# Optimization experiments

Hardware: AMD Instinct MI355X
Metric: run time of the kernel (lower is better)

## Reference

```python
import jax, jax.numpy as jnp
import numpy as np

N = 10000
E = 160000
UNITS = 64
NUM_RBF = 32
CUTOFF = 1.0


def _xavier(k, shape):
    fan_out, fan_in = shape
    lim = float(np.sqrt(6.0 / (fan_in + fan_out)))
    return jax.random.uniform(k, shape, minval=-lim, maxval=lim, dtype=jnp.float32)


def setup_inputs() -> dict:
    key = jax.random.key(0)
    ks = jax.random.split(key, 16)
    inp = {
        "edge_index": jax.random.randint(ks[0], (2, E), 0, N),
        "edge_weight": jax.random.uniform(ks[1], (E,), dtype=jnp.float32),
        "edge_attr": jax.random.normal(ks[2], (E, NUM_RBF), dtype=jnp.float32),
        "X": jax.random.normal(ks[3], (N, UNITS, 3, 3), dtype=jnp.float32),
        # scalar MLP: num_rbf -> units -> 2*units -> 3*units
        "Ws0": _xavier(ks[4], (UNITS, NUM_RBF)), "bs0": jnp.zeros((UNITS,), jnp.float32),
        "Ws1": _xavier(ks[5], (2 * UNITS, UNITS)), "bs1": jnp.zeros((2 * UNITS,), jnp.float32),
        "Ws2": _xavier(ks[6], (3 * UNITS, 2 * UNITS)), "bs2": jnp.zeros((3 * UNITS,), jnp.float32),
    }
    for i in range(6):
        inp[f"Wt{i}"] = _xavier(ks[7 + i], (UNITS, UNITS))
    return inp


def cosine_cutoff(r, cutoff):
    return jnp.where(r < cutoff, 0.5 * (jnp.cos(jnp.pi * r / cutoff) + 1.0), 0.0)


def tensor_norm(X):
    # X: [N, units, 3, 3] -> [N, units]
    return jnp.sum(X * X, axis=(-2, -1))


def decompose_tensor(X):
    eye = jnp.eye(3, dtype=X.dtype)
    trace = jnp.trace(X, axis1=-2, axis2=-1)  # [N, units]
    I = (trace / 3.0)[..., None, None] * eye
    A = 0.5 * (X - jnp.swapaxes(X, -2, -1))
    S = 0.5 * (X + jnp.swapaxes(X, -2, -1)) - I
    return I, A, S


def channel_linear(T, W):
    # linear over the channel dim: [N, c, 3, 3] x [d, c] -> [N, d, 3, 3]
    return jnp.einsum('ncij,dc->ndij', T, W)


def reference(edge_index, edge_weight, edge_attr, X,
              Ws0, bs0, Ws1, bs1, Ws2, bs2,
              Wt0, Wt1, Wt2, Wt3, Wt4, Wt5):
    act = jax.nn.silu
    C = cosine_cutoff(edge_weight, CUTOFF)  # [E]
    h = act(edge_attr @ Ws0.T + bs0)
    h = act(h @ Ws1.T + bs1)
    h = act(h @ Ws2.T + bs2)  # [E, 3*units]
    ea = (h * C[:, None]).reshape(h.shape[0], UNITS, 3)  # [E, units, 3]

    X = X / (tensor_norm(X) + 1.0)[..., None, None]
    I, A, S = decompose_tensor(X)
    I = channel_linear(I, Wt0)
    A = channel_linear(A, Wt1)
    S = channel_linear(S, Wt2)
    Y = I + A + S

    src, dst = edge_index[0], edge_index[1]
    n = X.shape[0]
    # message = per-edge radial scaling of gathered node tensors; aggregate at src
    Im = jax.ops.segment_sum(ea[..., 0, None, None] * I[dst], src, num_segments=n)
    Am = jax.ops.segment_sum(ea[..., 1, None, None] * A[dst], src, num_segments=n)
    Sm = jax.ops.segment_sum(ea[..., 2, None, None] * S[dst], src, num_segments=n)
    msg = Im + Am + Sm

    # O(3): symmetrized product of batched 3x3 matmuls
    AB = jnp.matmul(msg, Y) + jnp.matmul(Y, msg)
    I2, A2, S2 = decompose_tensor(AB)
    normp1 = (tensor_norm(I2 + A2 + S2) + 1.0)[..., None, None]
    I2 = channel_linear(I2 / normp1, Wt3)
    A2 = channel_linear(A2 / normp1, Wt4)
    S2 = channel_linear(S2 / normp1, Wt5)
    dX = I2 + A2 + S2
    return X + dX + jnp.matmul(dX, dX)
```

## Files before the change

### kernel.cpp

```cpp
#include <hip/hip_runtime.h>
#include <math.h>

#define NN 10000
#define EE 160000

#define OFF_WTT 0
#define OFF_PK  24576
#define OFF_B2P 41984
#define OFF_IASH 42176
#define OFF_EAH 3882176
#define OFF_INT 19242176

typedef __attribute__((ext_vector_type(8))) _Float16 h16x8;
typedef __attribute__((ext_vector_type(2))) __fp16 fp16x2_raw;
typedef __attribute__((ext_vector_type(4))) float f32x4;

__device__ __forceinline__ float silu_f(float x) {
    return x * __builtin_amdgcn_rcpf(1.0f + __expf(-x));
}
__device__ __forceinline__ unsigned int pkh(float a, float b) {
    union { fp16x2_raw h; unsigned int u; } cv;
    cv.h = __builtin_amdgcn_cvt_pkrtz(a, b);
    return cv.u;
}
__device__ __forceinline__ unsigned short f2h(float f) {
    union { _Float16 h; unsigned short u; } cv; cv.h = (_Float16)f; return cv.u;
}
__device__ __forceinline__ float h2f(unsigned short s) {
    union { unsigned short u; _Float16 h; } cv; cv.u = s; return (float)cv.h;
}
__device__ __forceinline__ float h2f_lo(unsigned int u) { return h2f((unsigned short)(u & 0xffffu)); }
__device__ __forceinline__ float h2f_hi(unsigned int u) { return h2f((unsigned short)(u >> 16)); }

__global__ void k_prep(const float* __restrict__ Wt0, const float* __restrict__ Wt1,
                       const float* __restrict__ Wt2, const float* __restrict__ Wt3,
                       const float* __restrict__ Wt4, const float* __restrict__ Wt5,
                       const float* __restrict__ Ws0, const float* __restrict__ Ws1,
                       const float* __restrict__ Ws2, const float* __restrict__ bs2,
                       const int* __restrict__ ei,
                       float* __restrict__ WtT, unsigned short* __restrict__ PK,
                       float* __restrict__ bs2p, int* __restrict__ counts) {
    int idx = blockIdx.x * 256 + threadIdx.x;
    if (idx < 24576) {
        int k = idx >> 12, r = idx & 4095;
        int c = r >> 6, d = r & 63;
        const float* W = (k == 0) ? Wt0 : (k == 1) ? Wt1 : (k == 2) ? Wt2
                       : (k == 3) ? Wt3 : (k == 4) ? Wt4 : Wt5;
        WtT[idx] = W[d * 64 + c];
    } else if (idx < 26624) {
        int q = idx - 24576;
        int ot = q >> 9, r = q & 511, lane = r >> 3, j = r & 7;
        int k = ((lane >> 4) * 8) + j, o = ot * 16 + (lane & 15);
        PK[q] = f2h(Ws0[o * 32 + k]);
    } else if (idx < 34816) {
        int q = idx - 24576;
        int i = q - 2048, ch = i >> 9, r = i & 511, lane = r >> 3, j = r & 7;
        int ot = ch >> 1, ks = ch & 1;
        int k = ks * 32 + (lane >> 4) * 8 + j, o = ot * 16 + (lane & 15);
        PK[q] = f2h(Ws1[o * 64 + k]);
    } else if (idx < 59392) {
        int q = idx - 24576;
        int i = q - 10240, ch = i >> 9, r = i & 511, lane = r >> 3, j = r & 7;
        int ot = ch >> 2, ks = ch & 3;
        int k = ks * 32 + (lane >> 4) * 8 + j;
        int op = ot * 16 + (lane & 15);
        int o = (op & 63) * 3 + (op >> 6);
        PK[q] = f2h(Ws2[o * 128 + k]);
    } else if (idx < 59584) {
        int op = idx - 59392;
        bs2p[op] = bs2[(op & 63) * 3 + (op >> 6)];
    } else if (idx < 59584 + EE) {
        int e = idx - 59584;
        atomicAdd(&counts[ei[e]], 1);
    }
}

__global__ __launch_bounds__(256) void k_scan(const int* __restrict__ counts,
                                              int* __restrict__ offsets) {
    __shared__ int sums[256];
    int t = threadIdx.x;
    const int CH = 40;
    int base = t * CH;
    int s = 0;
    for (int i = 0; i < CH; i++) {
        int idx = base + i;
        if (idx < NN) s += counts[idx];
    }
    sums[t] = s;
    __syncthreads();
    for (int off = 1; off < 256; off <<= 1) {
        int tmp = (t >= off) ? sums[t - off] : 0;
        __syncthreads();
        sums[t] += tmp;
        __syncthreads();
    }
    int run = sums[t] - s;
    for (int i = 0; i < CH; i++) {
        int idx = base + i;
        if (idx < NN) { offsets[idx] = run; run += counts[idx]; }
    }
    if (t == 255) offsets[NN] = run;
}

__global__ void k_fill(const int* __restrict__ ei, const int* __restrict__ offsets,
                       int* __restrict__ cursor, int* __restrict__ bucket,
                       int* __restrict__ dstp) {
    int e = blockIdx.x * 256 + threadIdx.x;
    if (e < EE) {
        int s = ei[e];
        int pos = offsets[s] + atomicAdd(&cursor[s], 1);
        bucket[pos] = e;
        dstp[pos] = ei[EE + e];
    }
}

__global__ __launch_bounds__(64) void k_nodeprep(const float* __restrict__ X,
                                                 const float* __restrict__ WtT,
                                                 unsigned short* __restrict__ IASh) {
    int n = blockIdx.x, c = threadIdx.x;
    __shared__ float XS[576];
    __shared__ float L[64][12];
#pragma unroll
    for (int i = 0; i < 9; i++) XS[c + 64 * i] = X[(size_t)n * 576 + c + 64 * i];
    __syncthreads();
    float x[9];
#pragma unroll
    for (int j = 0; j < 9; j++) x[j] = XS[c * 9 + j];
    float nrm = 0.f;
#pragma unroll
    for (int j = 0; j < 9; j++) nrm += x[j] * x[j];
    float inv = __builtin_amdgcn_rcpf(nrm + 1.0f);
#pragma unroll
    for (int j = 0; j < 9; j++) x[j] *= inv;
    float tr3 = (x[0] + x[4] + x[8]) * (1.0f / 3.0f);
    L[c][0] = tr3;
    L[c][1] = 0.5f * (x[1] - x[3]);
    L[c][2] = 0.5f * (x[2] - x[6]);
    L[c][3] = 0.5f * (x[5] - x[7]);
    L[c][4] = x[0] - tr3;
    L[c][5] = x[4] - tr3;
    L[c][6] = 0.5f * (x[1] + x[3]);
    L[c][7] = 0.5f * (x[2] + x[6]);
    L[c][8] = 0.5f * (x[5] + x[7]);
    __syncthreads();
    int d = c;
    const float* W0 = WtT;
    const float* W1 = WtT + 4096;
    const float* W2 = WtT + 8192;
    float aI = 0, aA0 = 0, aA1 = 0, aA2 = 0, aS0 = 0, aS1 = 0, aS2 = 0, aS3 = 0, aS4 = 0;
    for (int cc = 0; cc < 64; ++cc) {
        float w0 = W0[cc * 64 + d], w1 = W1[cc * 64 + d], w2 = W2[cc * 64 + d];
        float4 L0 = *(const float4*)&L[cc][0];
        float4 L1 = *(const float4*)&L[cc][4];
        float L8 = L[cc][8];
        aI  += w0 * L0.x;
        aA0 += w1 * L0.y; aA1 += w1 * L0.z; aA2 += w1 * L0.w;
        aS0 += w2 * L1.x; aS1 += w2 * L1.y; aS2 += w2 * L1.z;
        aS3 += w2 * L1.w; aS4 += w2 * L8;
    }
    unsigned int* op = (unsigned int*)(IASh + (size_t)n * 768 + (size_t)d * 12);
    op[0] = pkh(aI, aA0);
    op[1] = pkh(aA1, aA2);
    op[2] = pkh(aS0, aS1);
    op[3] = pkh(aS2, aS3);
    op[4] = pkh(aS4, 0.0f);
}

__global__ __launch_bounds__(256) void k_mlp(const float* __restrict__ attr,
                                             const float* __restrict__ ew,
                                             const int* __restrict__ bucket,
                                             const unsigned short* __restrict__ PK,
                                             const float* __restrict__ bs0,
                                             const float* __restrict__ bs1,
                                             const float* __restrict__ bs2p,
                                             unsigned short* __restrict__ eah) {
    __shared__ unsigned short H1[64][80];
    __shared__ unsigned short H2[64][144];
    int t = threadIdx.x;
    int e0 = blockIdx.x * 64;
    int l = t & 63, w = t >> 6, rb = w * 16, lr = l & 15, lg = l >> 4;
    int eid = bucket[e0 + rb + lr];
    const float* ap = attr + (size_t)eid * 32 + lg * 8;
    float4 av0 = *(const float4*)ap;
    float4 av1 = *(const float4*)(ap + 4);
    union { h16x8 h; unsigned int u[4]; } B1;
    B1.u[0] = pkh(av0.x, av0.y); B1.u[1] = pkh(av0.z, av0.w);
    B1.u[2] = pkh(av1.x, av1.y); B1.u[3] = pkh(av1.z, av1.w);
    float rw = ew[eid];
    float C = (rw < 1.0f) ? 0.5f * (cosf(3.14159265358979f * rw) + 1.0f) : 0.0f;

    const h16x8* P1 = (const h16x8*)PK;
    const h16x8* P2 = (const h16x8*)(PK + 2048);
    const h16x8* P3 = (const h16x8*)(PK + 10240);

#pragma unroll
    for (int ot = 0; ot < 4; ++ot) {
        float4 bb = *(const float4*)&bs0[ot * 16 + lg * 4];
        f32x4 acc = {bb.x, bb.y, bb.z, bb.w};
        acc = __builtin_amdgcn_mfma_f32_16x16x32_f16(P1[ot * 64 + l], B1.h, acc, 0, 0, 0);
        unsigned int u01 = pkh(silu_f(acc[0]), silu_f(acc[1]));
        unsigned int u23 = pkh(silu_f(acc[2]), silu_f(acc[3]));
        *(uint2*)&H1[rb + lr][ot * 16 + lg * 4] = make_uint2(u01, u23);
    }
    __syncthreads();

    h16x8 B2a = *(const h16x8*)&H1[rb + lr][lg * 8];
    h16x8 B2b = *(const h16x8*)&H1[rb + lr][32 + lg * 8];
#pragma unroll
    for (int ot = 0; ot < 8; ++ot) {
        float4 bb = *(const float4*)&bs1[ot * 16 + lg * 4];
        f32x4 acc = {bb.x, bb.y, bb.z, bb.w};
        acc = __builtin_amdgcn_mfma_f32_16x16x32_f16(P2[(ot * 2 + 0) * 64 + l], B2a, acc, 0, 0, 0);
        acc = __builtin_amdgcn_mfma_f32_16x16x32_f16(P2[(ot * 2 + 1) * 64 + l], B2b, acc, 0, 0, 0);
        unsigned int u01 = pkh(silu_f(acc[0]), silu_f(acc[1]));
        unsigned int u23 = pkh(silu_f(acc[2]), silu_f(acc[3]));
        *(uint2*)&H2[rb + lr][ot * 16 + lg * 4] = make_uint2(u01, u23);
    }
    __syncthreads();

    h16x8 B3[4];
#pragma unroll
    for (int ks = 0; ks < 4; ++ks)
        B3[ks] = *(const h16x8*)&H2[rb + lr][ks * 32 + lg * 8];
    size_t ebase = (size_t)(e0 + rb + lr) * 192;
#pragma unroll
    for (int ot = 0; ot < 12; ++ot) {
        float4 bb = *(const float4*)&bs2p[ot * 16 + lg * 4];
        f32x4 acc = {bb.x, bb.y, bb.z, bb.w};
#pragma unroll
        for (int ks = 0; ks < 4; ++ks)
            acc = __builtin_amdgcn_mfma_f32_16x16x32_f16(P3[(ot * 4 + ks) * 64 + l], B3[ks], acc, 0, 0, 0);
        unsigned int u01 = pkh(silu_f(acc[0]) * C, silu_f(acc[1]) * C);
        unsigned int u23 = pkh(silu_f(acc[2]) * C, silu_f(acc[3]) * C);
        *(uint2*)&eah[ebase + ot * 16 + lg * 4] = make_uint2(u01, u23);
    }
}

__global__ __launch_bounds__(64) void k_aggout(const int* __restrict__ offsets,
                                               const int* __restrict__ dstp,
                                               const unsigned short* __restrict__ eah,
                                               const unsigned short* __restrict__ IASh,
                                               const float* __restrict__ X,
                                               const float* __restrict__ WtT,
                                               float* __restrict__ out) {
    int n = blockIdx.x, c = threadIdx.x;
    __shared__ float XS[576];
    __shared__ float OS[576];
    __shared__ float L[64][12];
#pragma unroll
    for (int i = 0; i < 9; i++) XS[c + 64 * i] = X[(size_t)n * 576 + c + 64 * i];
    __syncthreads();

    int beg = offsets[n], end = offsets[n + 1];
    float m0 = 0, m1 = 0, m2 = 0, m3 = 0, m4 = 0, m5 = 0, m6 = 0, m7 = 0, m8 = 0;
    for (int i = beg; i < end; ++i) {
        int dst = dstp[i];
        const unsigned short* ep = eah + (size_t)i * 192;
        float ea0 = h2f(ep[c]), ea1 = h2f(ep[64 + c]), ea2 = h2f(ep[128 + c]);
        const unsigned int* ip = (const unsigned int*)(IASh + (size_t)dst * 768 + (size_t)c * 12);
        uint2 qa = *(const uint2*)ip;
        uint2 qb = *(const uint2*)(ip + 2);
        unsigned int qc = ip[4];
        m0 += ea0 * h2f_lo(qa.x); m1 += ea1 * h2f_hi(qa.x);
        m2 += ea1 * h2f_lo(qa.y); m3 += ea1 * h2f_hi(qa.y);
        m4 += ea2 * h2f_lo(qb.x); m5 += ea2 * h2f_hi(qb.x);
        m6 += ea2 * h2f_lo(qb.y); m7 += ea2 * h2f_hi(qb.y);
        m8 += ea2 * h2f_lo(qc);
    }
    const unsigned int* yp = (const unsigned int*)(IASh + (size_t)n * 768 + (size_t)c * 12);
    uint2 ya = *(const uint2*)yp;
    uint2 yb = *(const uint2*)(yp + 2);
    unsigned int yc = yp[4];
    float yI = h2f_lo(ya.x), yA0 = h2f_hi(ya.x), yA1 = h2f_lo(ya.y), yA2 = h2f_hi(ya.y);
    float yS0 = h2f_lo(yb.x), yS1 = h2f_hi(yb.x), yS2 = h2f_lo(yb.y), yS3 = h2f_hi(yb.y);
    float yS4 = h2f_lo(yc);

    float M[3][3] = {
        { m0 + m4,   m1 + m6,  m2 + m7 },
        { -m1 + m6,  m0 + m5,  m3 + m8 },
        { -m2 + m7, -m3 + m8,  m0 - m4 - m5 } };
    float Y[3][3] = {
        { yI + yS0,   yA0 + yS2,  yA1 + yS3 },
        { -yA0 + yS2, yI + yS1,   yA2 + yS4 },
        { -yA1 + yS3, -yA2 + yS4, yI - yS0 - yS1 } };
    float AB[3][3];
#pragma unroll
    for (int i = 0; i < 3; i++)
#pragma unroll
        for (int j = 0; j < 3; j++) {
            float s = 0.f;
#pragma unroll
            for (int k = 0; k < 3; k++) s += M[i][k] * Y[k][j] + Y[i][k] * M[k][j];
            AB[i][j] = s;
        }
    float tr3 = (AB[0][0] + AB[1][1] + AB[2][2]) * (1.0f / 3.0f);
    float fro = 0.f;
#pragma unroll
    for (int i = 0; i < 3; i++)
#pragma unroll
        for (int j = 0; j < 3; j++) fro += AB[i][j] * AB[i][j];
    float inv = __builtin_amdgcn_rcpf(fro + 1.0f);
    L[c][0] = tr3 * inv;
    L[c][1] = 0.5f * (AB[0][1] - AB[1][0]) * inv;
    L[c][2] = 0.5f * (AB[0][2] - AB[2][0]) * inv;
    L[c][3] = 0.5f * (AB[1][2] - AB[2][1]) * inv;
    L[c][4] = (AB[0][0] - tr3) * inv;
    L[c][5] = (AB[1][1] - tr3) * inv;
    L[c][6] = 0.5f * (AB[0][1] + AB[1][0]) * inv;
    L[c][7] = 0.5f * (AB[0][2] + AB[2][0]) * inv;
    L[c][8] = 0.5f * (AB[1][2] + AB[2][1]) * inv;
    __syncthreads();
    int d = c;
    const float* W3 = WtT + 3 * 4096;
    const float* W4 = WtT + 4 * 4096;
    const float* W5 = WtT + 5 * 4096;
    float aI = 0, aA0 = 0, aA1 = 0, aA2 = 0, aS0 = 0, aS1 = 0, aS2 = 0, aS3 = 0, aS4 = 0;
    for (int cc = 0; cc < 64; ++cc) {
        float w3 = W3[cc * 64 + d], w4 = W4[cc * 64 + d], w5 = W5[cc * 64 + d];
        float4 L0 = *(const float4*)&L[cc][0];
        float4 L1 = *(const float4*)&L[cc][4];
        float L8 = L[cc][8];
        aI  += w3 * L0.x;
        aA0 += w4 * L0.y; aA1 += w4 * L0.z; aA2 += w4 * L0.w;
        aS0 += w5 * L1.x; aS1 += w5 * L1.y; aS2 += w5 * L1.z;
        aS3 += w5 * L1.w; aS4 += w5 * L8;
    }
    float dX[3][3] = {
        { aI + aS0,   aA0 + aS2,  aA1 + aS3 },
        { -aA0 + aS2, aI + aS1,   aA2 + aS4 },
        { -aA1 + aS3, -aA2 + aS4, aI - aS0 - aS1 } };
    float D2[3][3];
#pragma unroll
    for (int i = 0; i < 3; i++)
#pragma unroll
        for (int j = 0; j < 3; j++) {
            float s = 0.f;
#pragma unroll
            for (int k = 0; k < 3; k++) s += dX[i][k] * dX[k][j];
            D2[i][j] = s;
        }
    float x[9];
#pragma unroll
    for (int j = 0; j < 9; j++) x[j] = XS[d * 9 + j];
    float nrm = 0.f;
#pragma unroll
    for (int j = 0; j < 9; j++) nrm += x[j] * x[j];
    float xinv = __builtin_amdgcn_rcpf(nrm + 1.0f);
#pragma unroll
    for (int i = 0; i < 3; i++)
#pragma unroll
        for (int j = 0; j < 3; j++)
            OS[d * 9 + i * 3 + j] = x[i * 3 + j] * xinv + dX[i][j] + D2[i][j];
    __syncthreads();
#pragma unroll
    for (int i = 0; i < 9; i++) out[(size_t)n * 576 + c + 64 * i] = OS[c + 64 * i];
}

extern "C" void kernel_launch(void* const* d_in, const int* in_sizes, int n_in,
                              void* d_out, int out_size, void* d_ws, size_t ws_size,
                              hipStream_t stream) {
    (void)in_sizes; (void)n_in; (void)out_size; (void)ws_size;
    const int* ei = (const int*)d_in[0];
    const float* ew = (const float*)d_in[1];
    const float* attr = (const float*)d_in[2];
    const float* X = (const float*)d_in[3];
    const float* Ws0 = (const float*)d_in[4];
    const float* bs0 = (const float*)d_in[5];
    const float* Ws1 = (const float*)d_in[6];
    const float* bs1 = (const float*)d_in[7];
    const float* Ws2 = (const float*)d_in[8];
    const float* bs2 = (const float*)d_in[9];
    const float* Wt0 = (const float*)d_in[10];
    const float* Wt1 = (const float*)d_in[11];
    const float* Wt2 = (const float*)d_in[12];
    const float* Wt3 = (const float*)d_in[13];
    const float* Wt4 = (const float*)d_in[14];
    const float* Wt5 = (const float*)d_in[15];
    float* ws = (float*)d_ws;
    int* ibase = (int*)(ws + OFF_INT);
    int* counts = ibase;
    int* cursor = ibase + NN;
    int* offsets = ibase + 2 * NN;
    int* bucket = ibase + 3 * NN + 1;
    int* dstp = bucket + EE;
    unsigned short* PK = (unsigned short*)(ws + OFF_PK);
    unsigned short* IASh = (unsigned short*)(ws + OFF_IASH);
    unsigned short* eah = (unsigned short*)(ws + OFF_EAH);

    (void)hipMemsetAsync(counts, 0, 2 * NN * sizeof(int), stream);
    k_prep<<<(59584 + EE + 255) / 256, 256, 0, stream>>>(
        Wt0, Wt1, Wt2, Wt3, Wt4, Wt5, Ws0, Ws1, Ws2, bs2, ei,
        ws, PK, ws + OFF_B2P, counts);
    k_scan<<<1, 256, 0, stream>>>(counts, offsets);
    k_fill<<<(EE + 255) / 256, 256, 0, stream>>>(ei, offsets, cursor, bucket, dstp);
    k_nodeprep<<<NN, 64, 0, stream>>>(X, ws, IASh);
    k_mlp<<<EE / 64, 256, 0, stream>>>(attr, ew, bucket, PK, bs0, bs1, ws + OFF_B2P, eah);
    k_aggout<<<NN, 64, 0, stream>>>(offsets, dstp, eah, IASh, X, ws, (float*)d_out);
}
```

Measured before the change: 185.7 us.

## Repack node tensors channel-major, pack four nodes per block, vectorize scan

The node-tensor buffer moves from a 12-half-per-channel stride to a channel-major layout of five packed words. Each gathered word is then read coalesced across the wave, and the buffer shrinks from 12 to 10 halves per channel. k_nodeprep and k_aggout now process four nodes per 256-thread block with one wave per node, using wave barriers in place of block syncs. k_mlp drops its block-wide syncs in favour of per-wave shared buffers, the aggregation loop is unrolled by two edges, and the scan reads counts as int4. The cost is more shared memory per block, and correctness now relies on wave-level barriers and on NN being divisible by four.

Result: faster. 162.8 us (-12.3%).

```diff
diff --git a/kernel.cpp b/kernel.cpp
--- a/kernel.cpp
+++ b/kernel.cpp
@@ -8,8 +8,8 @@
 #define OFF_PK  24576
 #define OFF_B2P 41984
 #define OFF_IASH 42176
-#define OFF_EAH 3882176
-#define OFF_INT 19242176
+#define OFF_EAH 3242176
+#define OFF_INT 18602176
 
 typedef __attribute__((ext_vector_type(8))) _Float16 h16x8;
 typedef __attribute__((ext_vector_type(2))) __fp16 fp16x2_raw;
@@ -79,12 +79,12 @@
                                               int* __restrict__ offsets) {
     __shared__ int sums[256];
     int t = threadIdx.x;
-    const int CH = 40;
-    int base = t * CH;
+    int base = t * 40;
     int s = 0;
-    for (int i = 0; i < CH; i++) {
-        int idx = base + i;
-        if (idx < NN) s += counts[idx];
+    if (base < NN) {
+        const int4* p = (const int4*)(counts + base);
+#pragma unroll
+        for (int q = 0; q < 10; ++q) { int4 a = p[q]; s += a.x + a.y + a.z + a.w; }
     }
     sums[t] = s;
     __syncthreads();
@@ -95,9 +95,16 @@
         __syncthreads();
     }
     int run = sums[t] - s;
-    for (int i = 0; i < CH; i++) {
-        int idx = base + i;
-        if (idx < NN) { offsets[idx] = run; run += counts[idx]; }
+    if (base < NN) {
+        const int4* p = (const int4*)(counts + base);
+#pragma unroll
+        for (int q = 0; q < 10; ++q) {
+            int4 a = p[q];
+            offsets[base + 4 * q + 0] = run; run += a.x;
+            offsets[base + 4 * q + 1] = run; run += a.y;
+            offsets[base + 4 * q + 2] = run; run += a.z;
+            offsets[base + 4 * q + 3] = run; run += a.w;
+        }
     }
     if (t == 255) offsets[NN] = run;
 }
@@ -114,18 +121,20 @@
     }
 }
 
-__global__ __launch_bounds__(64) void k_nodeprep(const float* __restrict__ X,
-                                                 const float* __restrict__ WtT,
-                                                 unsigned short* __restrict__ IASh) {
-    int n = blockIdx.x, c = threadIdx.x;
-    __shared__ float XS[576];
-    __shared__ float L[64][12];
-#pragma unroll
-    for (int i = 0; i < 9; i++) XS[c + 64 * i] = X[(size_t)n * 576 + c + 64 * i];
-    __syncthreads();
+__global__ __launch_bounds__(256) void k_nodeprep(const float* __restrict__ X,
+                                                  const float* __restrict__ WtT,
+                                                  unsigned int* __restrict__ IASu) {
+    int t = threadIdx.x, w = t >> 6, c = t & 63;
+    int n = blockIdx.x * 4 + w;
+    __shared__ float XS[4][576];
+    __shared__ float L[4][64][12];
+    float* xs = XS[w];
+#pragma unroll
+    for (int i = 0; i < 9; i++) xs[c + 64 * i] = X[(size_t)n * 576 + c + 64 * i];
+    __builtin_amdgcn_wave_barrier();
     float x[9];
 #pragma unroll
-    for (int j = 0; j < 9; j++) x[j] = XS[c * 9 + j];
+    for (int j = 0; j < 9; j++) x[j] = xs[c * 9 + j];
     float nrm = 0.f;
 #pragma unroll
     for (int j = 0; j < 9; j++) nrm += x[j] * x[j];
@@ -133,16 +142,16 @@
 #pragma unroll
     for (int j = 0; j < 9; j++) x[j] *= inv;
     float tr3 = (x[0] + x[4] + x[8]) * (1.0f / 3.0f);
-    L[c][0] = tr3;
-    L[c][1] = 0.5f * (x[1] - x[3]);
-    L[c][2] = 0.5f * (x[2] - x[6]);
-    L[c][3] = 0.5f * (x[5] - x[7]);
-    L[c][4] = x[0] - tr3;
-    L[c][5] = x[4] - tr3;
-    L[c][6] = 0.5f * (x[1] + x[3]);
-    L[c][7] = 0.5f * (x[2] + x[6]);
-    L[c][8] = 0.5f * (x[5] + x[7]);
-    __syncthreads();
+    L[w][c][0] = tr3;
+    L[w][c][1] = 0.5f * (x[1] - x[3]);
+    L[w][c][2] = 0.5f * (x[2] - x[6]);
+    L[w][c][3] = 0.5f * (x[5] - x[7]);
+    L[w][c][4] = x[0] - tr3;
+    L[w][c][5] = x[4] - tr3;
+    L[w][c][6] = 0.5f * (x[1] + x[3]);
+    L[w][c][7] = 0.5f * (x[2] + x[6]);
+    L[w][c][8] = 0.5f * (x[5] + x[7]);
+    __builtin_amdgcn_wave_barrier();
     int d = c;
     const float* W0 = WtT;
     const float* W1 = WtT + 4096;
@@ -150,20 +159,20 @@
     float aI = 0, aA0 = 0, aA1 = 0, aA2 = 0, aS0 = 0, aS1 = 0, aS2 = 0, aS3 = 0, aS4 = 0;
     for (int cc = 0; cc < 64; ++cc) {
         float w0 = W0[cc * 64 + d], w1 = W1[cc * 64 + d], w2 = W2[cc * 64 + d];
-        float4 L0 = *(const float4*)&L[cc][0];
-        float4 L1 = *(const float4*)&L[cc][4];
-        float L8 = L[cc][8];
+        float4 L0 = *(const float4*)&L[w][cc][0];
+        float4 L1 = *(const float4*)&L[w][cc][4];
+        float L8 = L[w][cc][8];
         aI  += w0 * L0.x;
         aA0 += w1 * L0.y; aA1 += w1 * L0.z; aA2 += w1 * L0.w;
         aS0 += w2 * L1.x; aS1 += w2 * L1.y; aS2 += w2 * L1.z;
         aS3 += w2 * L1.w; aS4 += w2 * L8;
     }
-    unsigned int* op = (unsigned int*)(IASh + (size_t)n * 768 + (size_t)d * 12);
-    op[0] = pkh(aI, aA0);
-    op[1] = pkh(aA1, aA2);
-    op[2] = pkh(aS0, aS1);
-    op[3] = pkh(aS2, aS3);
-    op[4] = pkh(aS4, 0.0f);
+    unsigned int* op = IASu + (size_t)n * 320 + d;
+    op[0]   = pkh(aI, aA0);
+    op[64]  = pkh(aA1, aA2);
+    op[128] = pkh(aS0, aS1);
+    op[192] = pkh(aS2, aS3);
+    op[256] = pkh(aS4, 0.0f);
 }
 
 __global__ __launch_bounds__(256) void k_mlp(const float* __restrict__ attr,
@@ -174,12 +183,11 @@
                                              const float* __restrict__ bs1,
                                              const float* __restrict__ bs2p,
                                              unsigned short* __restrict__ eah) {
-    __shared__ unsigned short H1[64][80];
-    __shared__ unsigned short H2[64][144];
+    __shared__ unsigned short H[4][16][152];
     int t = threadIdx.x;
-    int e0 = blockIdx.x * 64;
-    int l = t & 63, w = t >> 6, rb = w * 16, lr = l & 15, lg = l >> 4;
-    int eid = bucket[e0 + rb + lr];
+    int l = t & 63, w = t >> 6, lr = l & 15, lg = l >> 4;
+    int pos = blockIdx.x * 64 + w * 16 + lr;
+    int eid = bucket[pos];
     const float* ap = attr + (size_t)eid * 32 + lg * 8;
     float4 av0 = *(const float4*)ap;
     float4 av1 = *(const float4*)(ap + 4);
@@ -200,12 +208,13 @@
         acc = __builtin_amdgcn_mfma_f32_16x16x32_f16(P1[ot * 64 + l], B1.h, acc, 0, 0, 0);
         unsigned int u01 = pkh(silu_f(acc[0]), silu_f(acc[1]));
         unsigned int u23 = pkh(silu_f(acc[2]), silu_f(acc[3]));
-        *(uint2*)&H1[rb + lr][ot * 16 + lg * 4] = make_uint2(u01, u23);
-    }
-    __syncthreads();
-
-    h16x8 B2a = *(const h16x8*)&H1[rb + lr][lg * 8];
-    h16x8 B2b = *(const h16x8*)&H1[rb + lr][32 + lg * 8];
+        *(uint2*)&H[w][lr][ot * 16 + lg * 4] = make_uint2(u01, u23);
+    }
+    __builtin_amdgcn_wave_barrier();
+
+    h16x8 B2a = *(const h16x8*)&H[w][lr][lg * 8];
+    h16x8 B2b = *(const h16x8*)&H[w][lr][32 + lg * 8];
+    __builtin_amdgcn_wave_barrier();
 #pragma unroll
     for (int ot = 0; ot < 8; ++ot) {
         float4 bb = *(const float4*)&bs1[ot * 16 + lg * 4];
@@ -214,15 +223,15 @@
         acc = __builtin_amdgcn_mfma_f32_16x16x32_f16(P2[(ot * 2 + 1) * 64 + l], B2b, acc, 0, 0, 0);
         unsigned int u01 = pkh(silu_f(acc[0]), silu_f(acc[1]));
         unsigned int u23 = pkh(silu_f(acc[2]), silu_f(acc[3]));
-        *(uint2*)&H2[rb + lr][ot * 16 + lg * 4] = make_uint2(u01, u23);
-    }
-    __syncthreads();
+        *(uint2*)&H[w][lr][ot * 16 + lg * 4] = make_uint2(u01, u23);
+    }
+    __builtin_amdgcn_wave_barrier();
 
     h16x8 B3[4];
 #pragma unroll
     for (int ks = 0; ks < 4; ++ks)
-        B3[ks] = *(const h16x8*)&H2[rb + lr][ks * 32 + lg * 8];
-    size_t ebase = (size_t)(e0 + rb + lr) * 192;
+        B3[ks] = *(const h16x8*)&H[w][lr][ks * 32 + lg * 8];
+    size_t ebase = (size_t)pos * 192;
 #pragma unroll
     for (int ot = 0; ot < 12; ++ot) {
         float4 bb = *(const float4*)&bs2p[ot * 16 + lg * 4];
@@ -236,44 +245,62 @@
     }
 }
 
-__global__ __launch_bounds__(64) void k_aggout(const int* __restrict__ offsets,
-                                               const int* __restrict__ dstp,
-                                               const unsigned short* __restrict__ eah,
-                                               const unsigned short* __restrict__ IASh,
-                                               const float* __restrict__ X,
-                                               const float* __restrict__ WtT,
-                                               float* __restrict__ out) {
-    int n = blockIdx.x, c = threadIdx.x;
-    __shared__ float XS[576];
-    __shared__ float OS[576];
-    __shared__ float L[64][12];
-#pragma unroll
-    for (int i = 0; i < 9; i++) XS[c + 64 * i] = X[(size_t)n * 576 + c + 64 * i];
-    __syncthreads();
+__global__ __launch_bounds__(256) void k_aggout(const int* __restrict__ offsets,
+                                                const int* __restrict__ dstp,
+                                                const unsigned short* __restrict__ eah,
+                                                const unsigned int* __restrict__ IASu,
+                                                const float* __restrict__ X,
+                                                const float* __restrict__ WtT,
+                                                float* __restrict__ out) {
+    int t = threadIdx.x, w = t >> 6, c = t & 63;
+    int n = blockIdx.x * 4 + w;
+    __shared__ float XS[4][576];
+    __shared__ float LO[4][768];
+    float* xs = XS[w];
+    float* lo = LO[w];
+#pragma unroll
+    for (int i = 0; i < 9; i++) xs[c + 64 * i] = X[(size_t)n * 576 + c + 64 * i];
 
     int beg = offsets[n], end = offsets[n + 1];
     float m0 = 0, m1 = 0, m2 = 0, m3 = 0, m4 = 0, m5 = 0, m6 = 0, m7 = 0, m8 = 0;
-    for (int i = beg; i < end; ++i) {
-        int dst = dstp[i];
-        const unsigned short* ep = eah + (size_t)i * 192;
-        float ea0 = h2f(ep[c]), ea1 = h2f(ep[64 + c]), ea2 = h2f(ep[128 + c]);
-        const unsigned int* ip = (const unsigned int*)(IASh + (size_t)dst * 768 + (size_t)c * 12);
-        uint2 qa = *(const uint2*)ip;
-        uint2 qb = *(const uint2*)(ip + 2);
-        unsigned int qc = ip[4];
-        m0 += ea0 * h2f_lo(qa.x); m1 += ea1 * h2f_hi(qa.x);
-        m2 += ea1 * h2f_lo(qa.y); m3 += ea1 * h2f_hi(qa.y);
-        m4 += ea2 * h2f_lo(qb.x); m5 += ea2 * h2f_hi(qb.x);
-        m6 += ea2 * h2f_lo(qb.y); m7 += ea2 * h2f_hi(qb.y);
-        m8 += ea2 * h2f_lo(qc);
-    }
-    const unsigned int* yp = (const unsigned int*)(IASh + (size_t)n * 768 + (size_t)c * 12);
-    uint2 ya = *(const uint2*)yp;
-    uint2 yb = *(const uint2*)(yp + 2);
-    unsigned int yc = yp[4];
-    float yI = h2f_lo(ya.x), yA0 = h2f_hi(ya.x), yA1 = h2f_lo(ya.y), yA2 = h2f_hi(ya.y);
-    float yS0 = h2f_lo(yb.x), yS1 = h2f_hi(yb.x), yS2 = h2f_lo(yb.y), yS3 = h2f_hi(yb.y);
-    float yS4 = h2f_lo(yc);
+    int i = beg;
+    for (; i + 2 <= end; i += 2) {
+        int d0 = dstp[i], d1 = dstp[i + 1];
+        const unsigned short* ep0 = eah + (size_t)i * 192;
+        const unsigned short* ep1 = ep0 + 192;
+        float a00 = h2f(ep0[c]), a01 = h2f(ep0[64 + c]), a02 = h2f(ep0[128 + c]);
+        float a10 = h2f(ep1[c]), a11 = h2f(ep1[64 + c]), a12 = h2f(ep1[128 + c]);
+        const unsigned int* p0 = IASu + (size_t)d0 * 320 + c;
+        const unsigned int* p1 = IASu + (size_t)d1 * 320 + c;
+        unsigned int u00 = p0[0], u01 = p0[64], u02 = p0[128], u03 = p0[192], u04 = p0[256];
+        unsigned int u10 = p1[0], u11 = p1[64], u12 = p1[128], u13 = p1[192], u14 = p1[256];
+        m0 += a00 * h2f_lo(u00) + a10 * h2f_lo(u10);
+        m1 += a01 * h2f_hi(u00) + a11 * h2f_hi(u10);
+        m2 += a01 * h2f_lo(u01) + a11 * h2f_lo(u11);
+        m3 += a01 * h2f_hi(u01) + a11 * h2f_hi(u11);
+        m4 += a02 * h2f_lo(u02) + a12 * h2f_lo(u12);
+        m5 += a02 * h2f_hi(u02) + a12 * h2f_hi(u12);
+        m6 += a02 * h2f_lo(u03) + a12 * h2f_lo(u13);
+        m7 += a02 * h2f_hi(u03) + a12 * h2f_hi(u13);
+        m8 += a02 * h2f_lo(u04) + a12 * h2f_lo(u14);
+    }
+    if (i < end) {
+        int d0 = dstp[i];
+        const unsigned short* ep0 = eah + (size_t)i * 192;
+        float a00 = h2f(ep0[c]), a01 = h2f(ep0[64 + c]), a02 = h2f(ep0[128 + c]);
+        const unsigned int* p0 = IASu + (size_t)d0 * 320 + c;
+        unsigned int u00 = p0[0], u01 = p0[64], u02 = p0[128], u03 = p0[192], u04 = p0[256];
+        m0 += a00 * h2f_lo(u00); m1 += a01 * h2f_hi(u00);
+        m2 += a01 * h2f_lo(u01); m3 += a01 * h2f_hi(u01);
+        m4 += a02 * h2f_lo(u02); m5 += a02 * h2f_hi(u02);
+        m6 += a02 * h2f_lo(u03); m7 += a02 * h2f_hi(u03);
+        m8 += a02 * h2f_lo(u04);
+    }
+    const unsigned int* yp = IASu + (size_t)n * 320 + c;
+    unsigned int y0 = yp[0], y1 = yp[64], y2 = yp[128], y3 = yp[192], y4 = yp[256];
+    float yI = h2f_lo(y0), yA0 = h2f_hi(y0), yA1 = h2f_lo(y1), yA2 = h2f_hi(y1);
+    float yS0 = h2f_lo(y2), yS1 = h2f_hi(y2), yS2 = h2f_lo(y3), yS3 = h2f_hi(y3);
+    float yS4 = h2f_lo(y4);
 
     float M[3][3] = {
         { m0 + m4,   m1 + m6,  m2 + m7 },
@@ -285,31 +312,32 @@
         { -yA1 + yS3, -yA2 + yS4, yI - yS0 - yS1 } };
     float AB[3][3];
 #pragma unroll
-    for (int i = 0; i < 3; i++)
+    for (int ii = 0; ii < 3; ii++)
 #pragma unroll
         for (int j = 0; j < 3; j++) {
             float s = 0.f;
 #pragma unroll
-            for (int k = 0; k < 3; k++) s += M[i][k] * Y[k][j] + Y[i][k] * M[k][j];
-            AB[i][j] = s;
+            for (int k = 0; k < 3; k++) s += M[ii][k] * Y[k][j] + Y[ii][k] * M[k][j];
+            AB[ii][j] = s;
         }
     float tr3 = (AB[0][0] + AB[1][1] + AB[2][2]) * (1.0f / 3.0f);
     float fro = 0.f;
 #pragma unroll
-    for (int i = 0; i < 3; i++)
-#pragma unroll
-        for (int j = 0; j < 3; j++) fro += AB[i][j] * AB[i][j];
+    for (int ii = 0; ii < 3; ii++)
+#pragma unroll
+        for (int j = 0; j < 3; j++) fro += AB[ii][j] * AB[ii][j];
     float inv = __builtin_amdgcn_rcpf(fro + 1.0f);
-    L[c][0] = tr3 * inv;
-    L[c][1] = 0.5f * (AB[0][1] - AB[1][0]) * inv;
-    L[c][2] = 0.5f * (AB[0][2] - AB[2][0]) * inv;
-    L[c][3] = 0.5f * (AB[1][2] - AB[2][1]) * inv;
-    L[c][4] = (AB[0][0] - tr3) * inv;
-    L[c][5] = (AB[1][1] - tr3) * inv;
-    L[c][6] = 0.5f * (AB[0][1] + AB[1][0]) * inv;
-    L[c][7] = 0.5f * (AB[0][2] + AB[2][0]) * inv;
-    L[c][8] = 0.5f * (AB[1][2] + AB[2][1]) * inv;
-    __syncthreads();
+    float (*L12)[12] = (float (*)[12])lo;
+    L12[c][0] = tr3 * inv;
+    L12[c][1] = 0.5f * (AB[0][1] - AB[1][0]) * inv;
+    L12[c][2] = 0.5f * (AB[0][2] - AB[2][0]) * inv;
+    L12[c][3] = 0.5f * (AB[1][2] - AB[2][1]) * inv;
+    L12[c][4] = (AB[0][0] - tr3) * inv;
+    L12[c][5] = (AB[1][1] - tr3) * inv;
+    L12[c][6] = 0.5f * (AB[0][1] + AB[1][0]) * inv;
+    L12[c][7] = 0.5f * (AB[0][2] + AB[2][0]) * inv;
+    L12[c][8] = 0.5f * (AB[1][2] + AB[2][1]) * inv;
+    __builtin_amdgcn_wave_barrier();
     int d = c;
     const float* W3 = WtT + 3 * 4096;
     const float* W4 = WtT + 4 * 4096;
@@ -317,9 +345,9 @@
     float aI = 0, aA0 = 0, aA1 = 0, aA2 = 0, aS0 = 0, aS1 = 0, aS2 = 0, aS3 = 0, aS4 = 0;
     for (int cc = 0; cc < 64; ++cc) {
         float w3 = W3[cc * 64 + d], w4 = W4[cc * 64 + d], w5 = W5[cc * 64 + d];
-        float4 L0 = *(const float4*)&L[cc][0];
-        float4 L1 = *(const float4*)&L[cc][4];
-        float L8 = L[cc][8];
+        float4 L0 = *(const float4*)&L12[cc][0];
+        float4 L1 = *(const float4*)&L12[cc][4];
+        float L8 = L12[cc][8];
         aI  += w3 * L0.x;
         aA0 += w4 * L0.y; aA1 += w4 * L0.z; aA2 += w4 * L0.w;
         aS0 += w5 * L1.x; aS1 += w5 * L1.y; aS2 += w5 * L1.z;
@@ -331,29 +359,31 @@
         { -aA1 + aS3, -aA2 + aS4, aI - aS0 - aS1 } };
     float D2[3][3];
 #pragma unroll
-    for (int i = 0; i < 3; i++)
+    for (int ii = 0; ii < 3; ii++)
 #pragma unroll
         for (int j = 0; j < 3; j++) {
             float s = 0.f;
 #pragma unroll
-            for (int k = 0; k < 3; k++) s += dX[i][k] * dX[k][j];
-            D2[i][j] = s;
+            for (int k = 0; k < 3; k++) s += dX[ii][k] * dX[k][j];
+            D2[ii][j] = s;
         }
     float x[9];
-#pragma unroll
-    for (int j = 0; j < 9; j++) x[j] = XS[d * 9 + j];
+    __builtin_amdgcn_wave_barrier();
+#pragma unroll
+    for (int j = 0; j < 9; j++) x[j] = xs[d * 9 + j];
     float nrm = 0.f;
 #pragma unroll
     for (int j = 0; j < 9; j++) nrm += x[j] * x[j];
     float xinv = __builtin_amdgcn_rcpf(nrm + 1.0f);
-#pragma unroll
-    for (int i = 0; i < 3; i++)
+    __builtin_amdgcn_wave_barrier();
+#pragma unroll
+    for (int ii = 0; ii < 3; ii++)
 #pragma unroll
         for (int j = 0; j < 3; j++)
-            OS[d * 9 + i * 3 + j] = x[i * 3 + j] * xinv + dX[i][j] + D2[i][j];
-    __syncthreads();
-#pragma unroll
-    for (int i = 0; i < 9; i++) out[(size_t)n * 576 + c + 64 * i] = OS[c + 64 * i];
+            lo[d * 9 + ii * 3 + j] = x[ii * 3 + j] * xinv + dX[ii][j] + D2[ii][j];
+    __builtin_amdgcn_wave_barrier();
+#pragma unroll
+    for (int ii = 0; ii < 9; ii++) out[(size_t)n * 576 + c + 64 * ii] = lo[c + 64 * ii];
 }
 
 extern "C" void kernel_launch(void* const* d_in, const int* in_sizes, int n_in,
@@ -384,7 +414,7 @@
     int* bucket = ibase + 3 * NN + 1;
     int* dstp = bucket + EE;
     unsigned short* PK = (unsigned short*)(ws + OFF_PK);
-    unsigned short* IASh = (unsigned short*)(ws + OFF_IASH);
+    unsigned int* IASu = (unsigned int*)(ws + OFF_IASH);
     unsigned short* eah = (unsigned short*)(ws + OFF_EAH);
 
     (void)hipMemsetAsync(counts, 0, 2 * NN * sizeof(int), stream);
@@ -393,7 +423,7 @@
         ws, PK, ws + OFF_B2P, counts);
     k_scan<<<1, 256, 0, stream>>>(counts, offsets);
     k_fill<<<(EE + 255) / 256, 256, 0, stream>>>(ei, offsets, cursor, bucket, dstp);
-    k_nodeprep<<<NN, 64, 0, stream>>>(X, ws, IASh);
+    k_nodeprep<<<NN / 4, 256, 0, stream>>>(X, ws, IASu);
     k_mlp<<<EE / 64, 256, 0, stream>>>(attr, ew, bucket, PK, bs0, bs1, ws + OFF_B2P, eah);
-    k_aggout<<<NN, 64, 0, stream>>>(offsets, dstp, eah, IASh, X, ws, (float*)d_out);
-}
+    k_aggout<<<NN / 4, 256, 0, stream>>>(offsets, dstp, eah, IASu, X, ws, (float*)d_out);
+}
```
